# Performance work log

Measured on AMD Instinct MI355X. Metric: run time of the kernel, lower is better.

Reference implementation:

```python
import jax, jax.numpy as jnp
import numpy as np

B, T, D, H, N = 16, 512, 256, 4, 10
DK = D // H
EPS = 1e-12  # espnet LayerNorm eps


def _pe(t, d):
    # espnet PositionalEncoding table
    pos = np.arange(t, dtype=np.float32)[:, None]
    div = np.exp(np.arange(0, d, 2, dtype=np.float32) * (-np.log(10000.0) / d))
    pe = np.zeros((t, d), dtype=np.float32)
    pe[:, 0::2] = np.sin(pos * div)
    pe[:, 1::2] = np.cos(pos * div)
    return jnp.asarray(pe)


def _ln(x, g, b):
    m = jnp.mean(x, -1, keepdims=True)
    v = jnp.var(x, -1, keepdims=True)
    return (x - m) * jax.lax.rsqrt(v + EPS) * g + b


def _forward(x, x_lengths, lids, Wq, bq, Wk, bk, Wv, bv, Wo, bo, W1, b1, W2, b2, g1, be1, g2, be2, gf, bef):
    b, t, d = x.shape
    pe = _pe(t, d)
    pad = jnp.arange(t)[None, :] < x_lengths[:, None]          # [b,t] non-pad mask
    amask = pad[:, None, None, :]                               # [b,1,1,t] key mask
    onehot = (lids[:, None] == jnp.arange(N)[None, :]).astype(x.dtype)  # [b,N]
    h0 = x * np.float32(np.sqrt(d)) + pe[None]                  # scaled input + pos-enc (shared across experts)
    neg = jnp.finfo(x.dtype).min
    out = jnp.zeros_like(x)
    for z in range(N):  # fixed small set of structurally-distinct experts
        # pre-norm self-attention block
        hn = _ln(h0, g1[z], be1[z])
        q = (hn @ Wq[z] + bq[z]).reshape(b, t, H, DK).transpose(0, 2, 1, 3)
        k_ = (hn @ Wk[z] + bk[z]).reshape(b, t, H, DK).transpose(0, 2, 1, 3)
        v_ = (hn @ Wv[z] + bv[z]).reshape(b, t, H, DK).transpose(0, 2, 1, 3)
        scores = jnp.einsum('bhqd,bhkd->bhqk', q, k_) / np.float32(np.sqrt(DK))
        attn = jax.nn.softmax(jnp.where(amask, scores, neg), axis=-1)
        attn = jnp.where(amask, attn, jnp.zeros((), x.dtype))
        ctx = jnp.einsum('bhqk,bhkd->bhqd', attn, v_).transpose(0, 2, 1, 3).reshape(b, t, d)
        h = h0 + ctx @ Wo[z] + bo[z]
        # pre-norm feed-forward block
        hn2 = _ln(h, g2[z], be2[z])
        h = h + jax.nn.relu(hn2 @ W1[z] + b1[z]) @ W2[z] + b2[z]
        # final after_norm, then one-hot masked combine (== emb_lang sum)
        out = out + onehot[:, z, None, None] * _ln(h, gf[z], bef[z])
    return out


def setup_inputs() -> dict:
    key = jax.random.key(0)
    ks = jax.random.split(key, 12)
    s = np.float32(0.02)
    FF = 4 * D
    return {
        'x': jax.random.normal(ks[0], (B, T, D), jnp.float32),
        'x_lengths': jax.random.randint(ks[1], (B,), T // 2, T + 1),
        'lids': jax.random.randint(ks[2], (B,), 0, N),
        'Wq': jax.random.normal(ks[3], (N, D, D), jnp.float32) * s,
        'bq': jnp.zeros((N, D), jnp.float32),
        'Wk': jax.random.normal(ks[4], (N, D, D), jnp.float32) * s,
        'bk': jnp.zeros((N, D), jnp.float32),
        'Wv': jax.random.normal(ks[5], (N, D, D), jnp.float32) * s,
        'bv': jnp.zeros((N, D), jnp.float32),
        'Wo': jax.random.normal(ks[6], (N, D, D), jnp.float32) * s,
        'bo': jnp.zeros((N, D), jnp.float32),
        'W1': jax.random.normal(ks[7], (N, D, FF), jnp.float32) * s,
        'b1': jnp.zeros((N, FF), jnp.float32),
        'W2': jax.random.normal(ks[8], (N, FF, D), jnp.float32) * s,
        'b2': jnp.zeros((N, D), jnp.float32),
        'g1': jnp.ones((N, D), jnp.float32),
        'be1': jnp.zeros((N, D), jnp.float32),
        'g2': jnp.ones((N, D), jnp.float32),
        'be2': jnp.zeros((N, D), jnp.float32),
        'gf': jnp.ones((N, D), jnp.float32),
        'bef': jnp.zeros((N, D), jnp.float32),
    }


def reference(x, x_lengths, lids, Wq, bq, Wk, bk, Wv, bv, Wo, bo, W1, b1, W2, b2, g1, be1, g2, be2, gf, bef):
    return _forward(x, x_lengths, lids, Wq, bq, Wk, bk, Wv, bv, Wo, bo, W1, b1, W2, b2, g1, be1, g2, be2, gf, bef)
```

## Files before the change

kernel.cpp:

```cpp
#include <hip/hip_runtime.h>

typedef unsigned short u16;
typedef __bf16 bf16x8 __attribute__((ext_vector_type(8)));
typedef float  f32x4  __attribute__((ext_vector_type(4)));
typedef unsigned int   u32x4 __attribute__((ext_vector_type(4)));
typedef unsigned short u16x4 __attribute__((ext_vector_type(4)));

#define DEV __device__ __forceinline__

#define NB   16
#define TT   512
#define DD   256
#define HH   4
#define DKH  64
#define NLANG 10
#define FFD  1024

DEV u16 f2bf(float f) {
  unsigned int u = __builtin_bit_cast(unsigned int, f);
  return (u16)((u + 0x7fffu + ((u >> 16) & 1u)) >> 16);
}

DEV f32x4 zero4() { f32x4 z; z[0]=0.f; z[1]=0.f; z[2]=0.f; z[3]=0.f; return z; }

typedef __attribute__((address_space(1))) const unsigned int g_as1;
typedef __attribute__((address_space(3))) unsigned int l_as3;
DEV void load_lds16(const void* g, void* l) {
  __builtin_amdgcn_global_load_lds((g_as1*)g, (l_as3*)l, 16, 0, 0);
}

DEV bf16x8 lds_frag(const u16* lds, int row, int slot) {
  return *(const bf16x8*)(lds + row * 64 + ((slot ^ (row & 7)) << 3));
}

__global__ __launch_bounds__(256) void pre_kernel(
    const float* __restrict__ Wq, const float* __restrict__ Wk,
    const float* __restrict__ Wv, const float* __restrict__ Wo,
    const float* __restrict__ W1, const float* __restrict__ W2,
    u16* __restrict__ wtq, u16* __restrict__ wtk, u16* __restrict__ wtv,
    u16* __restrict__ wto, u16* __restrict__ wt1, u16* __restrict__ wt2,
    const float* __restrict__ x, float* __restrict__ h0, u16* __restrict__ hn,
    const float* __restrict__ g, const float* __restrict__ be,
    const int* __restrict__ lids) {
  __shared__ u16 tile[64][33];
  const int bx = blockIdx.x;
  if (bx < 3840) {
    const float* src; u16* dst; int R, C, z, r0, c0;
    if (bx < 1280) {
      const int w = bx / 320, rem = bx % 320;
      src = (w == 0) ? Wq : (w == 1) ? Wk : (w == 2) ? Wv : Wo;
      dst = (w == 0) ? wtq : (w == 1) ? wtk : (w == 2) ? wtv : wto;
      R = 256; C = 256; z = rem >> 5;
      const int rc = rem & 31; r0 = (rc >> 3) * 64; c0 = (rc & 7) * 32;
    } else if (bx < 2560) {
      const int rem = bx - 1280; src = W1; dst = wt1; R = 256; C = 1024;
      z = rem >> 7; const int rc = rem & 127; r0 = (rc >> 5) * 64; c0 = (rc & 31) * 32;
    } else {
      const int rem = bx - 2560; src = W2; dst = wt2; R = 1024; C = 256;
      z = rem >> 7; const int rc = rem & 127; r0 = (rc >> 3) * 64; c0 = (rc & 7) * 32;
    }
    bool used = false;
#pragma unroll
    for (int i = 0; i < NB; ++i) used |= (lids[i] == z);
    if (!used) return;
    const float* s = src + (size_t)z * R * C;
    u16* d = dst + (size_t)z * R * C;
    const int tx = threadIdx.x & 31, ty = threadIdx.x >> 5;
#pragma unroll
    for (int rr = 0; rr < 8; ++rr) {
      const int r = ty + rr * 8;
      tile[r][tx] = f2bf(s[(size_t)(r0 + r) * C + c0 + tx]);
    }
    __syncthreads();
#pragma unroll
    for (int rr = 0; rr < 4; ++rr) {
      const int cc = ty + rr * 8;
      const unsigned int lo = tile[tx * 2][cc], hi = tile[tx * 2 + 1][cc];
      *(unsigned int*)(d + (size_t)(c0 + cc) * R + r0 + tx * 2) = lo | (hi << 16);
    }
  } else {
    const int wave = threadIdx.x >> 6, lane = threadIdx.x & 63;
    const int row = (bx - 3840) * 4 + wave;
    const int b = row >> 9, t = row & 511;
    const int z = lids[b];
    const int c0 = lane * 4;
    const float4 xv = *(const float4*)(x + (size_t)row * DD + c0);
    const float kPE = -9.21034037197618f / 256.0f;
    float div0 = __expf(kPE * (float)c0);
    float div1 = __expf(kPE * (float)(c0 + 2));
    float a0 = div0 * (float)t, a1 = div1 * (float)t;
    float h[4];
    h[0] = xv.x * 16.0f + sinf(a0);
    h[1] = xv.y * 16.0f + cosf(a0);
    h[2] = xv.z * 16.0f + sinf(a1);
    h[3] = xv.w * 16.0f + cosf(a1);
    float s = h[0] + h[1] + h[2] + h[3];
    float ss = h[0]*h[0] + h[1]*h[1] + h[2]*h[2] + h[3]*h[3];
#pragma unroll
    for (int d = 1; d < 64; d <<= 1) { s += __shfl_xor(s, d); ss += __shfl_xor(ss, d); }
    float mean = s * (1.0f / 256.0f);
    float var  = ss * (1.0f / 256.0f) - mean * mean;
    float rstd = rsqrtf(var + 1e-12f);
    *(float4*)(h0 + (size_t)row * DD + c0) = make_float4(h[0], h[1], h[2], h[3]);
    u16x4 o;
#pragma unroll
    for (int j = 0; j < 4; ++j)
      o[j] = f2bf((h[j] - mean) * rstd * g[z * DD + c0 + j] + be[z * DD + c0 + j]);
    *(u16x4*)(hn + (size_t)row * DD + c0) = o;
  }
}

DEV void gemm_tile(const u16* __restrict__ A, const u16* __restrict__ W, int K,
                   int m0, int n0, u16* Alds, u16* Blds, f32x4 acc[4][4]) {
  const int tid = threadIdx.x;
  const int lane = tid & 63;
  const int wave = tid >> 6;
  const int wm = wave >> 1, wn = wave & 1;
  const int l15 = lane & 15, lhi = lane >> 4;
  const int lr = lane >> 3, lsl = lane & 7;
  const u16* srcA[4]; const u16* srcB[4];
#pragma unroll
  for (int j = 0; j < 4; ++j) {
    const int r = wave * 32 + j * 8 + lr;
    srcA[j] = A + (size_t)(m0 + r) * K + ((lsl ^ (r & 7)) << 3);
    srcB[j] = W + (size_t)(n0 + r) * K + ((lsl ^ (r & 7)) << 3);
  }
  for (int k0 = 0; k0 < K; k0 += 64) {
#pragma unroll
    for (int j = 0; j < 4; ++j) {
      load_lds16(srcA[j] + k0, Alds + (wave * 32 + j * 8) * 64);
      load_lds16(srcB[j] + k0, Blds + (wave * 32 + j * 8) * 64);
    }
    __syncthreads();
#pragma unroll
    for (int ks = 0; ks < 2; ++ks) {
      const int slot = ks * 4 + lhi;
      bf16x8 af[4], bfr[4];
#pragma unroll
      for (int m = 0; m < 4; ++m)
        af[m] = lds_frag(Alds, wm * 64 + m * 16 + l15, slot);
#pragma unroll
      for (int n = 0; n < 4; ++n)
        bfr[n] = lds_frag(Blds, wn * 64 + n * 16 + l15, slot);
#pragma unroll
      for (int m = 0; m < 4; ++m)
#pragma unroll
        for (int n = 0; n < 4; ++n)
          acc[m][n] = __builtin_amdgcn_mfma_f32_16x16x32_bf16(af[m], bfr[n], acc[m][n], 0, 0, 0);
    }
    __syncthreads();
  }
}

template<int EPI>
__global__ __launch_bounds__(256) void gemm_kernel(const u16* __restrict__ A,
                                                   const u16* __restrict__ Wt,
                                                   const float* __restrict__ bias,
                                                   void* __restrict__ outp,
                                                   const int* __restrict__ lids,
                                                   int N, int K) {
  __shared__ u16 Alds[128 * 64];
  __shared__ u16 Blds[128 * 64];
  const int b = blockIdx.z;
  const int z = lids[b];
  const int m0 = blockIdx.y * 128, n0 = blockIdx.x * 128;
  f32x4 acc[4][4];
#pragma unroll
  for (int i = 0; i < 4; ++i)
#pragma unroll
    for (int j = 0; j < 4; ++j) acc[i][j] = zero4();
  gemm_tile(A + (size_t)b * TT * K, Wt + (size_t)z * N * K, K, m0, n0, Alds, Blds, acc);
  const int lane = threadIdx.x & 63, wave = threadIdx.x >> 6;
  const int wm = wave >> 1, wn = wave & 1;
  const int l15 = lane & 15, lhi = lane >> 4;
  float bvv[4];
#pragma unroll
  for (int n = 0; n < 4; ++n) bvv[n] = bias[(size_t)z * N + n0 + wn * 64 + n * 16 + l15];
#pragma unroll
  for (int m = 0; m < 4; ++m) {
    const int grow = m0 + wm * 64 + m * 16 + lhi * 4;
#pragma unroll
    for (int n = 0; n < 4; ++n) {
      const int gcol = n0 + wn * 64 + n * 16 + l15;
#pragma unroll
      for (int r = 0; r < 4; ++r) {
        float v = acc[m][n][r] + bvv[n];
        size_t idx = (size_t)b * TT * N + (size_t)(grow + r) * N + gcol;
        if (EPI == 1) ((u16*)outp)[idx] = f2bf(v > 0.f ? v : 0.f);
        else ((u16*)outp)[idx] = f2bf(v);
      }
    }
  }
}

__global__ __launch_bounds__(256) void gemm_qkv(const u16* __restrict__ A,
                                                const u16* __restrict__ wtq,
                                                const u16* __restrict__ wtk,
                                                const u16* __restrict__ wtv,
                                                const float* __restrict__ bq,
                                                const float* __restrict__ bk,
                                                const float* __restrict__ bv,
                                                u16* __restrict__ qo,
                                                u16* __restrict__ ko,
                                                u16* __restrict__ vto,
                                                const int* __restrict__ lids) {
  __shared__ u16 Alds[128 * 64];
  __shared__ u16 Blds[128 * 64];
  const int b = blockIdx.z & 15, which = blockIdx.z >> 4;
  const int z = lids[b];
  const u16* W = (which == 0) ? wtq : (which == 1) ? wtk : wtv;
  const float* bias = (which == 0) ? bq : (which == 1) ? bk : bv;
  const int m0 = blockIdx.y * 128, n0 = blockIdx.x * 128;
  f32x4 acc[4][4];
#pragma unroll
  for (int i = 0; i < 4; ++i)
#pragma unroll
    for (int j = 0; j < 4; ++j) acc[i][j] = zero4();
  gemm_tile(A + (size_t)b * TT * DD, W + (size_t)z * DD * DD, DD, m0, n0, Alds, Blds, acc);
  const int lane = threadIdx.x & 63, wave = threadIdx.x >> 6;
  const int wm = wave >> 1, wn = wave & 1;
  const int l15 = lane & 15, lhi = lane >> 4;
  float bvv[4];
#pragma unroll
  for (int n = 0; n < 4; ++n) bvv[n] = bias[(size_t)z * DD + n0 + wn * 64 + n * 16 + l15];
  if (which < 2) {
    u16* out = (which == 0) ? qo : ko;
#pragma unroll
    for (int m = 0; m < 4; ++m) {
      const int grow = m0 + wm * 64 + m * 16 + lhi * 4;
#pragma unroll
      for (int n = 0; n < 4; ++n) {
        const int gcol = n0 + wn * 64 + n * 16 + l15;
#pragma unroll
        for (int r = 0; r < 4; ++r)
          out[(size_t)b * TT * DD + (size_t)(grow + r) * DD + gcol] = f2bf(acc[m][n][r] + bvv[n]);
      }
    }
  } else {
#pragma unroll
    for (int m = 0; m < 4; ++m) {
      const int grow = m0 + wm * 64 + m * 16 + lhi * 4;
#pragma unroll
      for (int n = 0; n < 4; ++n) {
        const int gcol = n0 + wn * 64 + n * 16 + l15;
        u16x4 pk;
#pragma unroll
        for (int r = 0; r < 4; ++r) pk[r] = f2bf(acc[m][n][r] + bvv[n]);
        *(u16x4*)(vto + (size_t)(b * HH + (gcol >> 6)) * DKH * TT + (size_t)(gcol & 63) * TT + grow) = pk;
      }
    }
  }
}

__global__ __launch_bounds__(256) void sgemm_p(const u16* __restrict__ q,
                                               const u16* __restrict__ k,
                                               u16* __restrict__ P,
                                               float* __restrict__ pl,
                                               const int* __restrict__ lens) {
  __shared__ u16 Alds[128 * 64];
  __shared__ u16 Blds[128 * 64];
  const int kt = blockIdx.x, qt = blockIdx.y, bh = blockIdx.z;
  const int b = bh >> 2, h = bh & 3;
  const int len = lens[b];
  const int m0 = qt * 128, n0 = kt * 128;
  u16* Pb = P + (size_t)bh * TT * TT;
  float* plb = pl + (size_t)bh * 8 * TT;
  const int tid = threadIdx.x;
  if (n0 >= len) {
    const int row = m0 + (tid >> 1);
    u16* dst = Pb + (size_t)row * TT + n0 + (tid & 1) * 64;
    u32x4 z4; z4[0] = 0u; z4[1] = 0u; z4[2] = 0u; z4[3] = 0u;
#pragma unroll
    for (int i = 0; i < 8; ++i) *(u32x4*)(dst + i * 8) = z4;
    plb[(kt * 2 + (tid >> 7)) * TT + m0 + (tid & 127)] = 0.f;
    return;
  }
  const int lane = tid & 63, wave = tid >> 6;
  const int wm = wave >> 1, wn = wave & 1;
  const int l15 = lane & 15, lhi = lane >> 4;
  const int lr = lane >> 3, lsl = lane & 7;
  const u16* qbase = q + (size_t)b * TT * DD + h * DKH;
  const u16* kbase = k + (size_t)b * TT * DD + h * DKH;
#pragma unroll
  for (int j = 0; j < 4; ++j) {
    const int r = wave * 32 + j * 8 + lr;
    load_lds16(qbase + (size_t)(m0 + r) * DD + ((lsl ^ (r & 7)) << 3), Alds + (wave * 32 + j * 8) * 64);
    load_lds16(kbase + (size_t)(n0 + r) * DD + ((lsl ^ (r & 7)) << 3), Blds + (wave * 32 + j * 8) * 64);
  }
  __syncthreads();
  f32x4 acc[4][4];
#pragma unroll
  for (int i = 0; i < 4; ++i)
#pragma unroll
    for (int j = 0; j < 4; ++j) acc[i][j] = zero4();
#pragma unroll
  for (int ks = 0; ks < 2; ++ks) {
    const int slot = ks * 4 + lhi;
    bf16x8 af[4], bfr[4];
#pragma unroll
    for (int m = 0; m < 4; ++m)
      af[m] = lds_frag(Alds, wm * 64 + m * 16 + l15, slot);
#pragma unroll
    for (int n = 0; n < 4; ++n)
      bfr[n] = lds_frag(Blds, wn * 64 + n * 16 + l15, slot);
#pragma unroll
    for (int m = 0; m < 4; ++m)
#pragma unroll
      for (int n = 0; n < 4; ++n)
        acc[m][n] = __builtin_amdgcn_mfma_f32_16x16x32_bf16(af[m], bfr[n], acc[m][n], 0, 0, 0);
  }
  const float SC = 0.125f * 1.4426950408889634f;
  float lsum[4][4];
#pragma unroll
  for (int m = 0; m < 4; ++m)
#pragma unroll
    for (int r = 0; r < 4; ++r) lsum[m][r] = 0.f;
#pragma unroll
  for (int m = 0; m < 4; ++m) {
    const int grow = m0 + wm * 64 + m * 16 + lhi * 4;
#pragma unroll
    for (int n = 0; n < 4; ++n) {
      const int gcol = n0 + wn * 64 + n * 16 + l15;
      const bool in = gcol < len;
#pragma unroll
      for (int r = 0; r < 4; ++r) {
        float p = exp2f(acc[m][n][r] * SC);
        p = in ? p : 0.f;
        lsum[m][r] += p;
        Pb[(size_t)(grow + r) * TT + gcol] = (u16)(__builtin_bit_cast(unsigned int, p) >> 16);
      }
    }
  }
#pragma unroll
  for (int d = 1; d < 16; d <<= 1)
#pragma unroll
    for (int m = 0; m < 4; ++m)
#pragma unroll
      for (int r = 0; r < 4; ++r) lsum[m][r] += __shfl_xor(lsum[m][r], d);
  if (l15 == 0) {
#pragma unroll
    for (int m = 0; m < 4; ++m)
#pragma unroll
      for (int r = 0; r < 4; ++r)
        plb[(kt * 2 + wn) * TT + m0 + wm * 64 + m * 16 + lhi * 4 + r] = lsum[m][r];
  }
}

__global__ __launch_bounds__(256) void pv_norm(const u16* __restrict__ P,
                                               const float* __restrict__ pl,
                                               const u16* __restrict__ vt,
                                               u16* __restrict__ ctx) {
  __shared__ u16 Alds[128 * 64];
  __shared__ u16 Blds[64 * 64];
  const int qt = blockIdx.x, bh = blockIdx.y;
  const int b = bh >> 2, h = bh & 3;
  const int m0 = qt * 128;
  const int tid = threadIdx.x, lane = tid & 63, wave = tid >> 6;
  const int l15 = lane & 15, lhi = lane >> 4;
  const int lr = lane >> 3, lsl = lane & 7;
  const u16* Pb = P + (size_t)bh * TT * TT;
  const u16* vtb = vt + (size_t)bh * DKH * TT;
  const float* plb = pl + (size_t)bh * 8 * TT;
  const u16* srcA[4]; const u16* srcB[2];
#pragma unroll
  for (int j = 0; j < 4; ++j) {
    const int r = wave * 32 + j * 8 + lr;
    srcA[j] = Pb + (size_t)(m0 + r) * TT + ((lsl ^ (r & 7)) << 3);
  }
#pragma unroll
  for (int j = 0; j < 2; ++j) {
    const int r = wave * 16 + j * 8 + lr;
    srcB[j] = vtb + (size_t)r * TT + ((lsl ^ (r & 7)) << 3);
  }
  f32x4 acc[2][4];
#pragma unroll
  for (int i = 0; i < 2; ++i)
#pragma unroll
    for (int j = 0; j < 4; ++j) acc[i][j] = zero4();
  for (int k0 = 0; k0 < TT; k0 += 64) {
#pragma unroll
    for (int j = 0; j < 4; ++j)
      load_lds16(srcA[j] + k0, Alds + (wave * 32 + j * 8) * 64);
#pragma unroll
    for (int j = 0; j < 2; ++j)
      load_lds16(srcB[j] + k0, Blds + (wave * 16 + j * 8) * 64);
    __syncthreads();
#pragma unroll
    for (int ks = 0; ks < 2; ++ks) {
      const int slot = ks * 4 + lhi;
      bf16x8 af[2], bfr[4];
#pragma unroll
      for (int m = 0; m < 2; ++m)
        af[m] = lds_frag(Alds, wave * 32 + m * 16 + l15, slot);
#pragma unroll
      for (int n = 0; n < 4; ++n)
        bfr[n] = lds_frag(Blds, n * 16 + l15, slot);
#pragma unroll
      for (int m = 0; m < 2; ++m)
#pragma unroll
        for (int n = 0; n < 4; ++n)
          acc[m][n] = __builtin_amdgcn_mfma_f32_16x16x32_bf16(af[m], bfr[n], acc[m][n], 0, 0, 0);
    }
    __syncthreads();
  }
  u16* cb = ctx + (size_t)b * TT * DD + h * DKH;
#pragma unroll
  for (int m = 0; m < 2; ++m) {
#pragma unroll
    for (int r = 0; r < 4; ++r) {
      const int grow = m0 + wave * 32 + m * 16 + lhi * 4 + r;
      float rs = 0.f;
#pragma unroll
      for (int s = 0; s < 8; ++s) rs += plb[s * TT + grow];
      const float linv = 1.0f / rs;
#pragma unroll
      for (int n = 0; n < 4; ++n)
        cb[(size_t)grow * DD + n * 16 + l15] = f2bf(acc[m][n][r] * linv);
    }
  }
}

template<int FINAL>
__global__ __launch_bounds__(512) void gemm_ln_kernel(
    const u16* __restrict__ A, const u16* __restrict__ Wt,
    const float* __restrict__ bias, const float* __restrict__ res,
    float* __restrict__ outf, u16* __restrict__ outbf,
    const float* __restrict__ g, const float* __restrict__ be,
    const int* __restrict__ lids, int K) {
  __shared__ u16 Alds[32 * 64];
  __shared__ u16 Blds[256 * 64];
  __shared__ float Sred[2][4][16];
  __shared__ float SSred[2][4][16];
  const int b = blockIdx.y;
  const int z = lids[b];
  const int m0 = blockIdx.x * 32;
  const int tid = threadIdx.x, lane = tid & 63, wave = tid >> 6;
  const int l15 = lane & 15, lhi = lane >> 4;
  const int lr = lane >> 3, lsl = lane & 7;
  const u16* Ab = A + (size_t)b * TT * K;
  const u16* Wb = Wt + (size_t)z * 256 * K;
  const u16* srcA = Ab;
  if (wave < 4) {
    const int rA = wave * 8 + lr;
    srcA = Ab + (size_t)(m0 + rA) * K + ((lsl ^ (rA & 7)) << 3);
  }
  const u16* srcB[4];
#pragma unroll
  for (int j = 0; j < 4; ++j) {
    const int rB = wave * 32 + j * 8 + lr;
    srcB[j] = Wb + (size_t)rB * K + ((lsl ^ (rB & 7)) << 3);
  }
  f32x4 acc[4];
#pragma unroll
  for (int n = 0; n < 4; ++n) acc[n] = zero4();
  for (int k0 = 0; k0 < K; k0 += 64) {
    if (wave < 4) load_lds16(srcA + k0, Alds + (wave * 8) * 64);
#pragma unroll
    for (int j = 0; j < 4; ++j)
      load_lds16(srcB[j] + k0, Blds + (wave * 32 + j * 8) * 64);
    __syncthreads();
#pragma unroll
    for (int ks = 0; ks < 2; ++ks) {
      const int slot = ks * 4 + lhi;
      bf16x8 af = lds_frag(Alds, (wave >> 2) * 16 + l15, slot);
#pragma unroll
      for (int n = 0; n < 4; ++n) {
        bf16x8 bf = lds_frag(Blds, (wave & 3) * 64 + n * 16 + l15, slot);
        acc[n] = __builtin_amdgcn_mfma_f32_16x16x32_bf16(af, bf, acc[n], 0, 0, 0);
      }
    }
    __syncthreads();
  }
  const int rbase = m0 + (wave >> 2) * 16;
  const int cq = (wave & 3) * 64;
  float bv[4], gv[4], bev[4];
#pragma unroll
  for (int n = 0; n < 4; ++n) {
    const int col = cq + n * 16 + l15;
    bv[n]  = bias[(size_t)z * 256 + col];
    gv[n]  = g[(size_t)z * 256 + col];
    bev[n] = be[(size_t)z * 256 + col];
  }
  float v[4][4];
  float sr[4] = {0.f, 0.f, 0.f, 0.f}, ssr[4] = {0.f, 0.f, 0.f, 0.f};
#pragma unroll
  for (int n = 0; n < 4; ++n) {
#pragma unroll
    for (int r = 0; r < 4; ++r) {
      const size_t idx = ((size_t)b * TT + rbase + lhi * 4 + r) * 256 + cq + n * 16 + l15;
      float t = acc[n][r] + bv[n] + res[idx];
      v[n][r] = t;
      sr[r] += t;
      ssr[r] += t * t;
    }
  }
#pragma unroll
  for (int d = 1; d < 16; d <<= 1)
#pragma unroll
    for (int r = 0; r < 4; ++r) { sr[r] += __shfl_xor(sr[r], d); ssr[r] += __shfl_xor(ssr[r], d); }
  if (l15 == 0) {
#pragma unroll
    for (int r = 0; r < 4; ++r) {
      Sred[wave >> 2][wave & 3][lhi * 4 + r] = sr[r];
      SSred[wave >> 2][wave & 3][lhi * 4 + r] = ssr[r];
    }
  }
  __syncthreads();
#pragma unroll
  for (int r = 0; r < 4; ++r) {
    float tot = 0.f, tss = 0.f;
#pragma unroll
    for (int qd = 0; qd < 4; ++qd) {
      tot += Sred[wave >> 2][qd][lhi * 4 + r];
      tss += SSred[wave >> 2][qd][lhi * 4 + r];
    }
    const float mean = tot * (1.0f / 256.0f);
    const float var  = tss * (1.0f / 256.0f) - mean * mean;
    const float rstd = rsqrtf(var + 1e-12f);
#pragma unroll
    for (int n = 0; n < 4; ++n) {
      const size_t idx = ((size_t)b * TT + rbase + lhi * 4 + r) * 256 + cq + n * 16 + l15;
      const float ln = (v[n][r] - mean) * rstd * gv[n] + bev[n];
      if (FINAL) {
        outf[idx] = ln;
      } else {
        outf[idx] = v[n][r];
        outbf[idx] = f2bf(ln);
      }
    }
  }
}

extern "C" void kernel_launch(void* const* d_in, const int* in_sizes, int n_in,
                              void* d_out, int out_size, void* d_ws, size_t ws_size,
                              hipStream_t stream) {
  (void)in_sizes; (void)n_in; (void)out_size; (void)ws_size;
  const float* x    = (const float*)d_in[0];
  const int*   xlen = (const int*)d_in[1];
  const int*   lids = (const int*)d_in[2];
  const float* Wq = (const float*)d_in[3];
  const float* bq = (const float*)d_in[4];
  const float* Wk = (const float*)d_in[5];
  const float* bk = (const float*)d_in[6];
  const float* Wv = (const float*)d_in[7];
  const float* bv = (const float*)d_in[8];
  const float* Wo = (const float*)d_in[9];
  const float* bo = (const float*)d_in[10];
  const float* W1 = (const float*)d_in[11];
  const float* b1 = (const float*)d_in[12];
  const float* W2 = (const float*)d_in[13];
  const float* b2 = (const float*)d_in[14];
  const float* g1 = (const float*)d_in[15];
  const float* be1= (const float*)d_in[16];
  const float* g2 = (const float*)d_in[17];
  const float* be2= (const float*)d_in[18];
  const float* gf = (const float*)d_in[19];
  const float* bef= (const float*)d_in[20];

  char* ws = (char*)d_ws;
  size_t off = 0;
  auto alloc = [&](size_t bytes) -> void* {
    void* p = ws + off;
    off = (off + bytes + 255) & ~(size_t)255;
    return p;
  };
  u16* wtq = (u16*)alloc((size_t)NLANG * DD * DD * 2);
  u16* wtk = (u16*)alloc((size_t)NLANG * DD * DD * 2);
  u16* wtv = (u16*)alloc((size_t)NLANG * DD * DD * 2);
  u16* wto = (u16*)alloc((size_t)NLANG * DD * DD * 2);
  u16* wt1 = (u16*)alloc((size_t)NLANG * DD * FFD * 2);
  u16* wt2 = (u16*)alloc((size_t)NLANG * FFD * DD * 2);
  float* h0 = (float*)alloc((size_t)NB * TT * DD * 4);
  float* hc = (float*)alloc((size_t)NB * TT * DD * 4);
  u16* hn  = (u16*)alloc((size_t)NB * TT * DD * 2);
  u16* qb  = (u16*)alloc((size_t)NB * TT * DD * 2);
  u16* kb  = (u16*)alloc((size_t)NB * TT * DD * 2);
  u16* vtb = (u16*)alloc((size_t)NB * TT * DD * 2);
  u16* ctx = (u16*)alloc((size_t)NB * TT * DD * 2);
  u16* Pm  = (u16*)alloc((size_t)NB * HH * TT * TT * 2);
  float* pl = (float*)alloc((size_t)NB * HH * 8 * TT * 4);
  u16* ffn = (u16*)alloc((size_t)NB * TT * FFD * 2);

  pre_kernel<<<dim3(3840 + 2048), 256, 0, stream>>>(
      Wq, Wk, Wv, Wo, W1, W2, wtq, wtk, wtv, wto, wt1, wt2,
      x, h0, hn, g1, be1, lids);

  gemm_qkv<<<dim3(2, 4, 48), 256, 0, stream>>>(hn, wtq, wtk, wtv, bq, bk, bv, qb, kb, vtb, lids);

  sgemm_p<<<dim3(4, 4, 64), 256, 0, stream>>>(qb, kb, Pm, pl, xlen);
  pv_norm<<<dim3(4, 64), 256, 0, stream>>>(Pm, pl, vtb, ctx);

  gemm_ln_kernel<0><<<dim3(16, NB), 512, 0, stream>>>(ctx, wto, bo, h0, hc, hn, g2, be2, lids, DD);

  gemm_kernel<1><<<dim3(8, 4, NB), 256, 0, stream>>>(hn, wt1, b1, ffn, lids, FFD, DD);

  gemm_ln_kernel<1><<<dim3(16, NB), 512, 0, stream>>>(ffn, wt2, b2, hc, (float*)d_out, nullptr, gf, bef, lids, FFD);
}
```

Measured before the change: 92.89 us.

## Fuse score, softmax and PV into one flash-style attention kernel

```diff
diff --git a/kernel.cpp b/kernel.cpp
--- a/kernel.cpp
+++ b/kernel.cpp
@@ -252,170 +252,145 @@
   }
 }
 
-__global__ __launch_bounds__(256) void sgemm_p(const u16* __restrict__ q,
-                                               const u16* __restrict__ k,
-                                               u16* __restrict__ P,
-                                               float* __restrict__ pl,
-                                               const int* __restrict__ lens) {
-  __shared__ u16 Alds[128 * 64];
-  __shared__ u16 Blds[128 * 64];
-  const int kt = blockIdx.x, qt = blockIdx.y, bh = blockIdx.z;
+__global__ __launch_bounds__(256, 1) void attn_fused(const u16* __restrict__ q,
+                                                     const u16* __restrict__ k,
+                                                     const u16* __restrict__ vt,
+                                                     u16* __restrict__ ctx,
+                                                     const int* __restrict__ lens) {
+  __shared__ u16 Klds[128 * 64];
+  __shared__ u16 Vlds[64 * 128];
+  __shared__ u16 Plds[128 * 128];
+  __shared__ float Lred[2][128];
+  const int qt = blockIdx.x, bh = blockIdx.y;
   const int b = bh >> 2, h = bh & 3;
   const int len = lens[b];
-  const int m0 = qt * 128, n0 = kt * 128;
-  u16* Pb = P + (size_t)bh * TT * TT;
-  float* plb = pl + (size_t)bh * 8 * TT;
-  const int tid = threadIdx.x;
-  if (n0 >= len) {
-    const int row = m0 + (tid >> 1);
-    u16* dst = Pb + (size_t)row * TT + n0 + (tid & 1) * 64;
-    u32x4 z4; z4[0] = 0u; z4[1] = 0u; z4[2] = 0u; z4[3] = 0u;
-#pragma unroll
-    for (int i = 0; i < 8; ++i) *(u32x4*)(dst + i * 8) = z4;
-    plb[(kt * 2 + (tid >> 7)) * TT + m0 + (tid & 127)] = 0.f;
-    return;
-  }
-  const int lane = tid & 63, wave = tid >> 6;
+  const int nt = (len + 127) >> 7;
+  const int tid = threadIdx.x, lane = tid & 63, wave = tid >> 6;
   const int wm = wave >> 1, wn = wave & 1;
   const int l15 = lane & 15, lhi = lane >> 4;
   const int lr = lane >> 3, lsl = lane & 7;
-  const u16* qbase = q + (size_t)b * TT * DD + h * DKH;
-  const u16* kbase = k + (size_t)b * TT * DD + h * DKH;
-#pragma unroll
-  for (int j = 0; j < 4; ++j) {
-    const int r = wave * 32 + j * 8 + lr;
-    load_lds16(qbase + (size_t)(m0 + r) * DD + ((lsl ^ (r & 7)) << 3), Alds + (wave * 32 + j * 8) * 64);
-    load_lds16(kbase + (size_t)(n0 + r) * DD + ((lsl ^ (r & 7)) << 3), Blds + (wave * 32 + j * 8) * 64);
-  }
-  __syncthreads();
-  f32x4 acc[4][4];
-#pragma unroll
-  for (int i = 0; i < 4; ++i)
-#pragma unroll
-    for (int j = 0; j < 4; ++j) acc[i][j] = zero4();
-#pragma unroll
-  for (int ks = 0; ks < 2; ++ks) {
-    const int slot = ks * 4 + lhi;
-    bf16x8 af[4], bfr[4];
-#pragma unroll
-    for (int m = 0; m < 4; ++m)
-      af[m] = lds_frag(Alds, wm * 64 + m * 16 + l15, slot);
-#pragma unroll
-    for (int n = 0; n < 4; ++n)
-      bfr[n] = lds_frag(Blds, wn * 64 + n * 16 + l15, slot);
-#pragma unroll
-    for (int m = 0; m < 4; ++m)
-#pragma unroll
-      for (int n = 0; n < 4; ++n)
-        acc[m][n] = __builtin_amdgcn_mfma_f32_16x16x32_bf16(af[m], bfr[n], acc[m][n], 0, 0, 0);
-  }
+  const int m0 = qt * 128;
+  const u16* qb = q + (size_t)b * TT * DD + h * DKH;
+  const u16* kb = k + (size_t)b * TT * DD + h * DKH;
+  const u16* vtb = vt + (size_t)bh * DKH * TT;
   const float SC = 0.125f * 1.4426950408889634f;
-  float lsum[4][4];
+
+  bf16x8 qf[4][2];
 #pragma unroll
   for (int m = 0; m < 4; ++m)
 #pragma unroll
-    for (int r = 0; r < 4; ++r) lsum[m][r] = 0.f;
-#pragma unroll
-  for (int m = 0; m < 4; ++m) {
-    const int grow = m0 + wm * 64 + m * 16 + lhi * 4;
-#pragma unroll
-    for (int n = 0; n < 4; ++n) {
-      const int gcol = n0 + wn * 64 + n * 16 + l15;
-      const bool in = gcol < len;
-#pragma unroll
-      for (int r = 0; r < 4; ++r) {
-        float p = exp2f(acc[m][n][r] * SC);
-        p = in ? p : 0.f;
-        lsum[m][r] += p;
-        Pb[(size_t)(grow + r) * TT + gcol] = (u16)(__builtin_bit_cast(unsigned int, p) >> 16);
-      }
-    }
-  }
-#pragma unroll
-  for (int d = 1; d < 16; d <<= 1)
-#pragma unroll
-    for (int m = 0; m < 4; ++m)
-#pragma unroll
-      for (int r = 0; r < 4; ++r) lsum[m][r] += __shfl_xor(lsum[m][r], d);
-  if (l15 == 0) {
-#pragma unroll
-    for (int m = 0; m < 4; ++m)
-#pragma unroll
-      for (int r = 0; r < 4; ++r)
-        plb[(kt * 2 + wn) * TT + m0 + wm * 64 + m * 16 + lhi * 4 + r] = lsum[m][r];
-  }
-}
-
-__global__ __launch_bounds__(256) void pv_norm(const u16* __restrict__ P,
-                                               const float* __restrict__ pl,
-                                               const u16* __restrict__ vt,
-                                               u16* __restrict__ ctx) {
-  __shared__ u16 Alds[128 * 64];
-  __shared__ u16 Blds[64 * 64];
-  const int qt = blockIdx.x, bh = blockIdx.y;
-  const int b = bh >> 2, h = bh & 3;
-  const int m0 = qt * 128;
-  const int tid = threadIdx.x, lane = tid & 63, wave = tid >> 6;
-  const int l15 = lane & 15, lhi = lane >> 4;
-  const int lr = lane >> 3, lsl = lane & 7;
-  const u16* Pb = P + (size_t)bh * TT * TT;
-  const u16* vtb = vt + (size_t)bh * DKH * TT;
-  const float* plb = pl + (size_t)bh * 8 * TT;
-  const u16* srcA[4]; const u16* srcB[2];
-#pragma unroll
-  for (int j = 0; j < 4; ++j) {
-    const int r = wave * 32 + j * 8 + lr;
-    srcA[j] = Pb + (size_t)(m0 + r) * TT + ((lsl ^ (r & 7)) << 3);
-  }
-#pragma unroll
-  for (int j = 0; j < 2; ++j) {
-    const int r = wave * 16 + j * 8 + lr;
-    srcB[j] = vtb + (size_t)r * TT + ((lsl ^ (r & 7)) << 3);
-  }
-  f32x4 acc[2][4];
+    for (int ks = 0; ks < 2; ++ks)
+      qf[m][ks] = *(const bf16x8*)(qb + (size_t)(m0 + wm * 64 + m * 16 + l15) * DD + ks * 32 + lhi * 8);
+
+  ((float*)Lred)[tid] = 0.f;
+
+  f32x4 oacc[2][4];
 #pragma unroll
   for (int i = 0; i < 2; ++i)
 #pragma unroll
-    for (int j = 0; j < 4; ++j) acc[i][j] = zero4();
-  for (int k0 = 0; k0 < TT; k0 += 64) {
-#pragma unroll
-    for (int j = 0; j < 4; ++j)
-      load_lds16(srcA[j] + k0, Alds + (wave * 32 + j * 8) * 64);
-#pragma unroll
-    for (int j = 0; j < 2; ++j)
-      load_lds16(srcB[j] + k0, Blds + (wave * 16 + j * 8) * 64);
-    __syncthreads();
+    for (int j = 0; j < 4; ++j) oacc[i][j] = zero4();
+
+  for (int kt = 0; kt < nt; ++kt) {
+#pragma unroll
+    for (int j = 0; j < 4; ++j) {
+      const int r = wave * 32 + j * 8 + lr;
+      load_lds16(kb + (size_t)(kt * 128 + r) * DD + ((lsl ^ (r & 7)) << 3),
+                 Klds + (wave * 32 + j * 8) * 64);
+    }
+#pragma unroll
+    for (int j = 0; j < 4; ++j) {
+      const int rv = wave * 16 + j * 4 + (lane >> 4);
+      const int cc = lane & 15;
+      load_lds16(vtb + (size_t)rv * TT + kt * 128 + ((cc ^ (rv & 7)) << 3),
+                 Vlds + (wave * 16 + j * 4) * 128);
+    }
+    __syncthreads();
+    f32x4 sacc[4][4];
+#pragma unroll
+    for (int i = 0; i < 4; ++i)
+#pragma unroll
+      for (int j = 0; j < 4; ++j) sacc[i][j] = zero4();
 #pragma unroll
     for (int ks = 0; ks < 2; ++ks) {
       const int slot = ks * 4 + lhi;
+      bf16x8 bfr[4];
+#pragma unroll
+      for (int n = 0; n < 4; ++n)
+        bfr[n] = lds_frag(Klds, wn * 64 + n * 16 + l15, slot);
+#pragma unroll
+      for (int m = 0; m < 4; ++m)
+#pragma unroll
+        for (int n = 0; n < 4; ++n)
+          sacc[m][n] = __builtin_amdgcn_mfma_f32_16x16x32_bf16(qf[m][ks], bfr[n], sacc[m][n], 0, 0, 0);
+    }
+    float lsum[4][4];
+#pragma unroll
+    for (int m = 0; m < 4; ++m)
+#pragma unroll
+      for (int r = 0; r < 4; ++r) lsum[m][r] = 0.f;
+#pragma unroll
+    for (int m = 0; m < 4; ++m) {
+#pragma unroll
+      for (int n = 0; n < 4; ++n) {
+        const int col = wn * 64 + n * 16 + l15;
+        const bool in = (kt * 128 + col) < len;
+#pragma unroll
+        for (int r = 0; r < 4; ++r) {
+          const int row = wm * 64 + m * 16 + lhi * 4 + r;
+          float p = exp2f(sacc[m][n][r] * SC);
+          p = in ? p : 0.f;
+          lsum[m][r] += p;
+          Plds[row * 128 + (col ^ ((row & 7) << 3))] = (u16)(__builtin_bit_cast(unsigned int, p) >> 16);
+        }
+      }
+    }
+#pragma unroll
+    for (int d = 1; d < 16; d <<= 1)
+#pragma unroll
+      for (int m = 0; m < 4; ++m)
+#pragma unroll
+        for (int r = 0; r < 4; ++r) lsum[m][r] += __shfl_xor(lsum[m][r], d);
+    if (l15 == 0) {
+#pragma unroll
+      for (int m = 0; m < 4; ++m)
+#pragma unroll
+        for (int r = 0; r < 4; ++r)
+          Lred[wn][wm * 64 + m * 16 + lhi * 4 + r] += lsum[m][r];
+    }
+    __syncthreads();
+#pragma unroll
+    for (int ks = 0; ks < 4; ++ks) {
+      const int cb = ks * 32 + lhi * 8;
       bf16x8 af[2], bfr[4];
 #pragma unroll
-      for (int m = 0; m < 2; ++m)
-        af[m] = lds_frag(Alds, wave * 32 + m * 16 + l15, slot);
+      for (int mm = 0; mm < 2; ++mm) {
+        const int row = wave * 32 + mm * 16 + l15;
+        af[mm] = *(const bf16x8*)(Plds + row * 128 + (cb ^ ((row & 7) << 3)));
+      }
+#pragma unroll
+      for (int n = 0; n < 4; ++n) {
+        const int row = n * 16 + l15;
+        bfr[n] = *(const bf16x8*)(Vlds + row * 128 + (cb ^ ((row & 7) << 3)));
+      }
+#pragma unroll
+      for (int mm = 0; mm < 2; ++mm)
+#pragma unroll
+        for (int n = 0; n < 4; ++n)
+          oacc[mm][n] = __builtin_amdgcn_mfma_f32_16x16x32_bf16(af[mm], bfr[n], oacc[mm][n], 0, 0, 0);
+    }
+    __syncthreads();
+  }
+
+  u16* cb2 = ctx + (size_t)b * TT * DD + h * DKH;
+#pragma unroll
+  for (int mm = 0; mm < 2; ++mm) {
+#pragma unroll
+    for (int r = 0; r < 4; ++r) {
+      const int row = wave * 32 + mm * 16 + lhi * 4 + r;
+      const float linv = 1.0f / (Lred[0][row] + Lred[1][row]);
 #pragma unroll
       for (int n = 0; n < 4; ++n)
-        bfr[n] = lds_frag(Blds, n * 16 + l15, slot);
-#pragma unroll
-      for (int m = 0; m < 2; ++m)
-#pragma unroll
-        for (int n = 0; n < 4; ++n)
-          acc[m][n] = __builtin_amdgcn_mfma_f32_16x16x32_bf16(af[m], bfr[n], acc[m][n], 0, 0, 0);
-    }
-    __syncthreads();
-  }
-  u16* cb = ctx + (size_t)b * TT * DD + h * DKH;
-#pragma unroll
-  for (int m = 0; m < 2; ++m) {
-#pragma unroll
-    for (int r = 0; r < 4; ++r) {
-      const int grow = m0 + wave * 32 + m * 16 + lhi * 4 + r;
-      float rs = 0.f;
-#pragma unroll
-      for (int s = 0; s < 8; ++s) rs += plb[s * TT + grow];
-      const float linv = 1.0f / rs;
-#pragma unroll
-      for (int n = 0; n < 4; ++n)
-        cb[(size_t)grow * DD + n * 16 + l15] = f2bf(acc[m][n][r] * linv);
+        cb2[(size_t)(m0 + row) * DD + n * 16 + l15] = f2bf(oacc[mm][n][r] * linv);
     }
   }
 }
@@ -577,8 +552,6 @@
   u16* kb  = (u16*)alloc((size_t)NB * TT * DD * 2);
   u16* vtb = (u16*)alloc((size_t)NB * TT * DD * 2);
   u16* ctx = (u16*)alloc((size_t)NB * TT * DD * 2);
-  u16* Pm  = (u16*)alloc((size_t)NB * HH * TT * TT * 2);
-  float* pl = (float*)alloc((size_t)NB * HH * 8 * TT * 4);
   u16* ffn = (u16*)alloc((size_t)NB * TT * FFD * 2);
 
   pre_kernel<<<dim3(3840 + 2048), 256, 0, stream>>>(
@@ -587,8 +560,7 @@
 
   gemm_qkv<<<dim3(2, 4, 48), 256, 0, stream>>>(hn, wtq, wtk, wtv, bq, bk, bv, qb, kb, vtb, lids);
 
-  sgemm_p<<<dim3(4, 4, 64), 256, 0, stream>>>(qb, kb, Pm, pl, xlen);
-  pv_norm<<<dim3(4, 64), 256, 0, stream>>>(Pm, pl, vtb, ctx);
+  attn_fused<<<dim3(4, 64), 256, 0, stream>>>(qb, kb, vtb, ctx, xlen);
 
   gemm_ln_kernel<0><<<dim3(16, NB), 512, 0, stream>>>(ctx, wto, bo, h0, hc, hn, g2, be2, lids, DD);
 
```

Measured after the change: 86.60 us. 1.07x faster.
